# Performance work log

Hardware: AMD Instinct MI355X
Metric: run time of the kernel (lower is better)

Reference implementation:

```python
import jax, jax.numpy as jnp
import numpy as np

DROPOUT = 0.2  # dropout radius in normalized [0,1] coords
EPS = 1e-08


def setup_inputs() -> dict:
    key = jax.random.key(0)
    k1, k2, k3, k4 = jax.random.split(key, 4)
    B, C, T = 64, 273, 3000
    brain_sig = jax.random.normal(k1, (B, C, T), dtype=jnp.float32)
    positions = jax.random.uniform(k2, (B, C, 2), dtype=jnp.float32)
    center = jax.random.uniform(k3, (2,), dtype=jnp.float32)
    mc_centers = jax.random.uniform(k4, (100, 2), dtype=jnp.float32)
    return {"brain_sig": brain_sig, "positions": positions,
            "center": center, "mc_centers": mc_centers}


def reference(brain_sig, positions, center, mc_centers):
    # kept channels: distance from ban center > dropout radius  -> (B, C)
    kept = jnp.linalg.norm(positions - center, axis=-1) > DROPOUT
    out = brain_sig * kept[:, :, None].astype(brain_sig.dtype)
    # Monte-Carlo estimate of keep probability (100 trials, vectorized)
    # diffs: (N, B, C, 2)
    diffs = positions[None, :, :, :] - mc_centers[:, None, None, :]
    kept_mc = jnp.linalg.norm(diffs, axis=-1) > DROPOUT  # (N, B, C)
    proba_kept = jnp.mean(kept_mc.astype(brain_sig.dtype), axis=0)  # (B, C)
    out = out / (EPS + proba_kept[:, :, None])
    return out
```

## Files before the change

### kernel.cpp

```cpp
#include <hip/hip_runtime.h>
#include <math.h>


__global__ __launch_bounds__(256) void channel_dropout_kernel(
    const float* __restrict__ sig,
    const float* __restrict__ pos,
    const float* __restrict__ center,
    const float* __restrict__ mc,
    float* __restrict__ out,
    int T, int NMC)
{
    const int row = blockIdx.x;
    const int t   = threadIdx.x;
    __shared__ float s_scale;

    if (t < 64) {
        const float px = pos[2 * row + 0];
        const float py = pos[2 * row + 1];
        float cnt = 0.0f;
        for (int i = t; i < NMC; i += 64) {
            const float dx = px - mc[2 * i + 0];
            const float dy = py - mc[2 * i + 1];
            cnt += (sqrtf(dx * dx + dy * dy) > 0.2f) ? 1.0f : 0.0f;
        }
        #pragma unroll
        for (int off = 32; off > 0; off >>= 1)
            cnt += __shfl_down(cnt, off, 64);
        if (t == 0) {
            const float dx = px - center[0];
            const float dy = py - center[1];
            const float kept =
                (sqrtf(dx * dx + dy * dy) > 0.2f) ? 1.0f : 0.0f;
            const float proba = cnt / (float)NMC;
            s_scale = kept / (1e-8f + proba);
        }
    }
    __syncthreads();
    const float scale = s_scale;

    const size_t base = (size_t)row * (size_t)T;
    const int n4 = T >> 2;
    const float4* __restrict__ in4  = (const float4*)(sig + base);
    float4* __restrict__       out4 = (float4*)(out + base);

    for (int i = t; i < n4; i += 256) {
        float4 v = in4[i];
        v.x *= scale; v.y *= scale; v.z *= scale; v.w *= scale;
        out4[i] = v;
    }
    for (int i = (n4 << 2) + t; i < T; i += 256) {
        out[base + i] = sig[base + i] * scale;
    }
}

extern "C" void kernel_launch(void* const* d_in, const int* in_sizes, int n_in,
                              void* d_out, int out_size, void* d_ws, size_t ws_size,
                              hipStream_t stream) {
    const float* sig    = (const float*)d_in[0];
    const float* pos    = (const float*)d_in[1];
    const float* center = (const float*)d_in[2];
    const float* mc     = (const float*)d_in[3];
    float* out          = (float*)d_out;

    const int rows = in_sizes[1] / 2;
    const int T    = in_sizes[0] / rows;
    const int NMC  = in_sizes[3] / 2;

    channel_dropout_kernel<<<rows, 256, 0, stream>>>(
        sig, pos, center, mc, out, T, NMC);
}
```

Baseline: 349.7 us.

## Split scale computation into separate kernel and stream multiple rows per block

Per-channel scale computation moves into its own kernel, which stages the MC centers in shared memory and gives one thread per channel, writing the scales to workspace. A separate streaming kernel then processes four rows per block as one contiguous range, using nontemporal vector loads and stores, so the per-block reduction and barrier disappear from the bandwidth-bound pass. The cost is an extra kernel launch, plus a global round-trip for the scales that makes the streaming pass wait on the scale kernel.

Result: no change. 352.5 us (+0.8%).

```diff
diff --git a/kernel.cpp b/kernel.cpp
--- a/kernel.cpp
+++ b/kernel.cpp
@@ -2,55 +2,84 @@
 #include <math.h>
 
 
-__global__ __launch_bounds__(256) void channel_dropout_kernel(
-    const float* __restrict__ sig,
+typedef float vfloat4 __attribute__((ext_vector_type(4)));
+
+__global__ __launch_bounds__(256) void scale_kernel(
     const float* __restrict__ pos,
     const float* __restrict__ center,
     const float* __restrict__ mc,
+    float* __restrict__ scales,
+    int rows, int NMC)
+{
+    extern __shared__ float s_mc[];
+    for (int i = threadIdx.x; i < 2 * NMC; i += blockDim.x)
+        s_mc[i] = mc[i];
+    __syncthreads();
+
+    const int row = blockIdx.x * blockDim.x + threadIdx.x;
+    if (row >= rows) return;
+
+    const float px = pos[2 * row + 0];
+    const float py = pos[2 * row + 1];
+
+    float cnt = 0.0f;
+    for (int j = 0; j < NMC; ++j) {
+        const float dx = px - s_mc[2 * j + 0];
+        const float dy = py - s_mc[2 * j + 1];
+        cnt += (sqrtf(dx * dx + dy * dy) > 0.2f) ? 1.0f : 0.0f;
+    }
+    const float proba = cnt / (float)NMC;
+
+    const float dx = px - center[0];
+    const float dy = py - center[1];
+    const float kept = (sqrtf(dx * dx + dy * dy) > 0.2f) ? 1.0f : 0.0f;
+
+    scales[row] = kept / (1e-8f + proba);
+}
+
+#define ROWS_PER_BLOCK 4
+
+__global__ __launch_bounds__(256) void stream_kernel(
+    const float* __restrict__ sig,
+    const float* __restrict__ scales,
     float* __restrict__ out,
-    int T, int NMC)
+    int n4_per_row,
+    int rows)
+{
+    const int r0 = blockIdx.x * ROWS_PER_BLOCK;
+    const int nr = min(ROWS_PER_BLOCK, rows - r0);
+
+    float s0 = scales[r0];
+    float s1 = (nr > 1) ? scales[r0 + 1] : 0.0f;
+    float s2 = (nr > 2) ? scales[r0 + 2] : 0.0f;
+    float s3 = (nr > 3) ? scales[r0 + 3] : 0.0f;
+
+    const size_t base4 = (size_t)r0 * (size_t)n4_per_row;
+    const int total4 = nr * n4_per_row;
+    const int n1 = n4_per_row, n2 = 2 * n4_per_row, n3 = 3 * n4_per_row;
+
+    const vfloat4* __restrict__ in4 = (const vfloat4*)sig + base4;
+    vfloat4* __restrict__ out4 = (vfloat4*)out + base4;
+
+    for (int i = threadIdx.x; i < total4; i += 256) {
+        const float sc = (i < n1) ? s0 : (i < n2) ? s1 : (i < n3) ? s2 : s3;
+        vfloat4 v = __builtin_nontemporal_load(in4 + i);
+        v *= sc;
+        __builtin_nontemporal_store(v, out4 + i);
+    }
+}
+
+__global__ __launch_bounds__(256) void tail_kernel(
+    const float* __restrict__ sig,
+    const float* __restrict__ scales,
+    float* __restrict__ out,
+    int T, int tail_start, int rows)
 {
     const int row = blockIdx.x;
-    const int t   = threadIdx.x;
-    __shared__ float s_scale;
-
-    if (t < 64) {
-        const float px = pos[2 * row + 0];
-        const float py = pos[2 * row + 1];
-        float cnt = 0.0f;
-        for (int i = t; i < NMC; i += 64) {
-            const float dx = px - mc[2 * i + 0];
-            const float dy = py - mc[2 * i + 1];
-            cnt += (sqrtf(dx * dx + dy * dy) > 0.2f) ? 1.0f : 0.0f;
-        }
-        #pragma unroll
-        for (int off = 32; off > 0; off >>= 1)
-            cnt += __shfl_down(cnt, off, 64);
-        if (t == 0) {
-            const float dx = px - center[0];
-            const float dy = py - center[1];
-            const float kept =
-                (sqrtf(dx * dx + dy * dy) > 0.2f) ? 1.0f : 0.0f;
-            const float proba = cnt / (float)NMC;
-            s_scale = kept / (1e-8f + proba);
-        }
-    }
-    __syncthreads();
-    const float scale = s_scale;
-
+    const float sc = scales[row];
     const size_t base = (size_t)row * (size_t)T;
-    const int n4 = T >> 2;
-    const float4* __restrict__ in4  = (const float4*)(sig + base);
-    float4* __restrict__       out4 = (float4*)(out + base);
-
-    for (int i = t; i < n4; i += 256) {
-        float4 v = in4[i];
-        v.x *= scale; v.y *= scale; v.z *= scale; v.w *= scale;
-        out4[i] = v;
-    }
-    for (int i = (n4 << 2) + t; i < T; i += 256) {
-        out[base + i] = sig[base + i] * scale;
-    }
+    for (int i = tail_start + (int)threadIdx.x; i < T; i += blockDim.x)
+        out[base + i] = sig[base + i] * sc;
 }
 
 extern "C" void kernel_launch(void* const* d_in, const int* in_sizes, int n_in,
@@ -61,11 +90,26 @@
     const float* center = (const float*)d_in[2];
     const float* mc     = (const float*)d_in[3];
     float* out          = (float*)d_out;
+    float* scales       = (float*)d_ws;
 
     const int rows = in_sizes[1] / 2;
     const int T    = in_sizes[0] / rows;
     const int NMC  = in_sizes[3] / 2;
 
-    channel_dropout_kernel<<<rows, 256, 0, stream>>>(
-        sig, pos, center, mc, out, T, NMC);
+    {
+        const int blocks = (rows + 255) / 256;
+        const size_t lds = (size_t)(2 * NMC) * sizeof(float);
+        scale_kernel<<<blocks, 256, lds, stream>>>(pos, center, mc, scales,
+                                                   rows, NMC);
+    }
+
+    {
+        const int n4 = T / 4;
+        const int blocks = (rows + ROWS_PER_BLOCK - 1) / ROWS_PER_BLOCK;
+        stream_kernel<<<blocks, 256, 0, stream>>>(sig, scales, out, n4, rows);
+        if (T % 4 != 0) {
+            tail_kernel<<<rows, 64, 0, stream>>>(sig, scales, out, T, n4 * 4,
+                                                 rows);
+        }
+    }
 }
```
